# Kernel tuning notes

Hardware: AMD Instinct MI355X
Metric: run time of the kernel (lower is better)

Reference implementation:

```python
import jax, jax.numpy as jnp
import numpy as np

ALPHA = 1.702
LIMIT = 7.0


def setup_inputs() -> dict:
    E, H, D = 16, 2880, 2880
    B, S = 2, 1024
    T = B * S
    key = jax.random.key(0)
    ks = jax.random.split(key, 8)
    hidden_states = jax.random.normal(ks[0], (B, S, H), dtype=jnp.float32)
    routing_weights = jax.random.uniform(ks[1], (T, E), dtype=jnp.float32)
    scale = 0.02
    Wg = jax.random.normal(ks[2], (E, H, D), dtype=jnp.float32) * scale
    bg = jax.random.normal(ks[3], (E, D), dtype=jnp.float32) * scale
    Wu = jax.random.normal(ks[4], (E, H, D), dtype=jnp.float32) * scale
    bu = jax.random.normal(ks[5], (E, D), dtype=jnp.float32) * scale
    Wd = jax.random.normal(ks[6], (E, D, H), dtype=jnp.float32) * scale
    bd = jax.random.normal(ks[7], (E, H), dtype=jnp.float32) * scale
    return {"hidden_states": hidden_states, "routing_weights": routing_weights,
            "Wg": Wg, "bg": bg, "Wu": Wu, "bu": bu, "Wd": Wd, "bd": bd}


def reference(hidden_states, routing_weights, Wg, bg, Wu, bu, Wd, bd):
    orig_shape = hidden_states.shape
    H = Wg.shape[1]
    x = hidden_states.reshape(-1, H)  # [T, H]
    # per-expert gate/up projections: [E, T, D]
    gate = jnp.einsum('th,ehd->etd', x, Wg) + bg[:, None, :]
    gate = jnp.minimum(gate, LIMIT)
    up = jnp.einsum('th,ehd->etd', x, Wu) + bu[:, None, :]
    up = jnp.clip(up, -LIMIT, LIMIT)
    glu = gate * jax.nn.sigmoid(gate * ALPHA)
    inter = (up + 1.0) * glu  # [E, T, D]
    # down projection: [E, T, H]
    down = jnp.einsum('etd,edh->eth', inter, Wd) + bd[:, None, :]
    # routing-weighted sum over experts: [T, H]
    out = jnp.einsum('eth,te->th', down, routing_weights)
    return out.reshape(orig_shape)
```

## Files before the change

### kernel.cpp

```cpp
#include <hip/hip_runtime.h>
#include <cstdint>


#define ALPHA 1.702f
#define LIMIT 7.0f

static constexpr int E = 16;
static constexpr int H = 2880;
static constexpr int D = 2880;
static constexpr int T = 2048;
static constexpr int NKT = H / 64;
static constexpr int NG  = 4;

typedef float        f32x4  __attribute__((ext_vector_type(4)));
typedef short        bf16x8 __attribute__((ext_vector_type(8)));

#define MFMA_BF16(a,b,c) __builtin_amdgcn_mfma_f32_16x16x32_bf16((a),(b),(c),0,0,0)
#define SBAR()        __builtin_amdgcn_s_barrier()
#define SCHED_FENCE() __builtin_amdgcn_sched_barrier(0)

__device__ __forceinline__ unsigned short f2bf(float f){
  unsigned u = __builtin_bit_cast(unsigned, f);
  u += 0x7fffu + ((u >> 16) & 1u);
  return (unsigned short)(u >> 16);
}
__device__ __forceinline__ unsigned pack2(float a, float b){
  return (unsigned)f2bf(a) | ((unsigned)f2bf(b) << 16);
}

__device__ __forceinline__ void gload_lds16(const void* g, void* l){
  __builtin_amdgcn_global_load_lds((const __attribute__((address_space(1))) unsigned*)g,
                                   (__attribute__((address_space(3))) unsigned*)l,
                                   16, 0, 0);
}

__global__ void cvt_kernel(const float* __restrict__ in, unsigned short* __restrict__ ob, int n8){
  int i = blockIdx.x * 256 + threadIdx.x;
  if (i < n8){
    float4 a = ((const float4*)in)[2*i];
    float4 b = ((const float4*)in)[2*i+1];
    uint4 o;
    o.x = pack2(a.x, a.y); o.y = pack2(a.z, a.w);
    o.z = pack2(b.x, b.y); o.w = pack2(b.z, b.w);
    ((uint4*)ob)[i] = o;
  }
}

__global__ __launch_bounds__(256) void tcvt_kernel(
    const float* __restrict__ src, unsigned short* __restrict__ dst)
{
  __shared__ unsigned short tl[64*72];
  const int t = threadIdx.x;
  const size_t mo = (size_t)blockIdx.z * H * D;
  const int r0 = blockIdx.x * 64, c0 = blockIdx.y * 64;
  const float* s = src + mo;
  unsigned short* o = dst + mo;

  int rr = t >> 2;
  #pragma unroll
  for (int p = 0; p < 4; ++p){
    int cc = ((t & 3) + p*4) * 4;
    float4 v = *(const float4*)(s + (size_t)(r0 + rr)*D + c0 + cc);
    tl[(cc+0)*72 + rr] = f2bf(v.x);
    tl[(cc+1)*72 + rr] = f2bf(v.y);
    tl[(cc+2)*72 + rr] = f2bf(v.z);
    tl[(cc+3)*72 + rr] = f2bf(v.w);
  }
  __syncthreads();
  #pragma unroll
  for (int p = 0; p < 2; ++p){
    int task = p*256 + t;
    int cl = task >> 3, ch = task & 7;
    bf16x8 v = *(const bf16x8*)&tl[cl*72 + ch*8];
    *(bf16x8*)(o + (size_t)(c0 + cl)*H + r0 + ch*8) = v;
  }
}

__global__ void reduce_kernel(const float* __restrict__ p, float* __restrict__ out, int n4){
  int i = blockIdx.x * 256 + threadIdx.x;
  if (i < n4){
    f32x4 a = ((const f32x4*)p)[i];
    #pragma unroll
    for (int g = 1; g < NG; ++g)
      a += ((const f32x4*)(p + (size_t)g * T * H))[i];
    ((f32x4*)out)[i] = a;
  }
}

__global__ __launch_bounds__(256, 2) void gateup_kernel(
    const unsigned short* __restrict__ xb,
    const unsigned short* __restrict__ wgT,
    const float* __restrict__ bg,
    const unsigned short* __restrict__ wuT,
    const float* __restrict__ bu,
    unsigned short* __restrict__ inter,
    int e0)
{
  __shared__ short As[2][128*64];
  __shared__ short Bg[2][96*64];
  __shared__ short Bu[2][96*64];

  const int t = threadIdx.x, lane = t & 63, wv = t >> 6;
  const int wm = wv >> 1, wn = wv & 1;

  int nbx = gridDim.x, nby = gridDim.y;
  int lin = blockIdx.x + nbx*(blockIdx.y + nby*blockIdx.z);
  int per = (nbx*nby*gridDim.z) >> 3;
  int id2 = (lin & 7)*per + (lin >> 3);
  int bx = id2 % nbx; int rem = id2 / nbx;
  int by = rem % nby; int bz = rem / nby;

  const int trow0 = bx * 128, ncol0 = by * 96, ez = bz, e = e0 + ez;
  const unsigned short* wg = wgT + (size_t)ez * D * H;
  const unsigned short* wu = wuT + (size_t)ez * D * H;

  f32x4 accg[4][3], accu[4][3];
  #pragma unroll
  for (int i = 0; i < 4; ++i)
    #pragma unroll
    for (int j = 0; j < 3; ++j){
      accg[i][j] = (f32x4){0.f,0.f,0.f,0.f};
      accu[i][j] = (f32x4){0.f,0.f,0.f,0.f};
    }

  auto stage = [&](int kt, int buf){
    #pragma unroll
    for (int i = 0; i < 4; ++i){
      int task = i*256 + t, row = task >> 3, ch = task & 7, sch = ch ^ (row & 7);
      gload_lds16(xb + (size_t)(trow0 + row)*H + kt*64 + sch*8, &As[buf][task*8]);
    }
    #pragma unroll
    for (int j = 0; j < 3; ++j){
      int task = j*256 + t, row = task >> 3, ch = task & 7, sch = ch ^ (row & 7);
      size_t go = (size_t)(ncol0 + row)*H + kt*64 + sch*8;
      gload_lds16(wg + go, &Bg[buf][task*8]);
      gload_lds16(wu + go, &Bu[buf][task*8]);
    }
  };

  stage(0, 0);

  for (int kt = 0; kt < NKT; ++kt){
    int cur = kt & 1, nxt = cur ^ 1;
    int ktn = (kt+1 < NKT) ? kt+1 : kt;
    stage(ktn, nxt);
    asm volatile("s_waitcnt vmcnt(10)" ::: "memory");
    SCHED_FENCE(); SBAR(); SCHED_FENCE();
    #pragma unroll
    for (int kk = 0; kk < 2; ++kk){
      bf16x8 af[4];
      #pragma unroll
      for (int mi = 0; mi < 4; ++mi){
        int row = wm*64 + mi*16 + (lane & 15);
        int pc  = (kk*4 + (lane>>4)) ^ (row & 7);
        af[mi] = *(const bf16x8*)&As[cur][row*64 + pc*8];
      }
      bf16x8 fgv[3], fuv[3];
      #pragma unroll
      for (int ni = 0; ni < 3; ++ni){
        int row = (wn*3 + ni)*16 + (lane & 15);
        int pc  = (kk*4 + (lane>>4)) ^ (row & 7);
        fgv[ni] = *(const bf16x8*)&Bg[cur][row*64 + pc*8];
        fuv[ni] = *(const bf16x8*)&Bu[cur][row*64 + pc*8];
      }
      #pragma unroll
      for (int ni = 0; ni < 3; ++ni)
        #pragma unroll
        for (int mi = 0; mi < 4; ++mi){
          accg[mi][ni] = MFMA_BF16(af[mi], fgv[ni], accg[mi][ni]);
          accu[mi][ni] = MFMA_BF16(af[mi], fuv[ni], accu[mi][ni]);
        }
    }
    SBAR();
  }
  asm volatile("s_waitcnt vmcnt(0)" ::: "memory");

  const float* bgp = bg + (size_t)e * D;
  const float* bup = bu + (size_t)e * D;
  unsigned short* ip = inter + (size_t)ez * T * D;
  #pragma unroll
  for (int ni = 0; ni < 3; ++ni){
    int d = ncol0 + wn*48 + ni*16 + (lane & 15);
    float bgv = bgp[d], buv = bup[d];
    #pragma unroll
    for (int mi = 0; mi < 4; ++mi){
      #pragma unroll
      for (int r = 0; r < 4; ++r){
        int trw = trow0 + wm*64 + mi*16 + (lane >> 4)*4 + r;
        float g = accg[mi][ni][r] + bgv;
        float u = accu[mi][ni][r] + buv;
        g = fminf(g, LIMIT);
        u = fminf(fmaxf(u, -LIMIT), LIMIT);
        float glu = g / (1.f + __expf(-ALPHA * g));
        ip[(size_t)trw * D + d] = f2bf((u + 1.f) * glu);
      }
    }
  }
}

__global__ __launch_bounds__(256, 2) void down_kernel(
    const unsigned short* __restrict__ inter,
    const unsigned short* __restrict__ wdT,
    const float* __restrict__ bd,
    const float* __restrict__ rw,
    float* __restrict__ pout,
    int e0, int ec)
{
  __shared__ short As[2][128*64];
  __shared__ short Bs[2][192*64];

  const int t = threadIdx.x, lane = t & 63, wv = t >> 6;
  const int wm = wv >> 1, wn = wv & 1;

  int nbx = gridDim.x, nby = gridDim.y;
  int lin = blockIdx.x + nbx*(blockIdx.y + nby*blockIdx.z);
  int per = (nbx*nby*gridDim.z) >> 3;
  int id2 = (lin & 7)*per + (lin >> 3);
  int bx = id2 % nbx; int rem = id2 / nbx;
  int by = rem % nby; int g  = rem / nby;

  const int trow0 = bx * 128, ncol0 = by * 192;
  const int ne = (ec > g) ? ((ec - 1 - g) >> 2) + 1 : 0;

  f32x4 oacc[4][6];
  #pragma unroll
  for (int i = 0; i < 4; ++i)
    #pragma unroll
    for (int j = 0; j < 6; ++j) oacc[i][j] = (f32x4){0.f,0.f,0.f,0.f};

  auto stage = [&](int ee, int kt, int buf){
    const unsigned short* ap = inter + (size_t)ee * T * D;
    const unsigned short* wd = wdT + (size_t)ee * H * D;
    #pragma unroll
    for (int i = 0; i < 4; ++i){
      int task = i*256 + t, row = task >> 3, ch = task & 7, sch = ch ^ (row & 7);
      gload_lds16(ap + (size_t)(trow0 + row)*D + kt*64 + sch*8, &As[buf][task*8]);
    }
    #pragma unroll
    for (int j = 0; j < 6; ++j){
      int task = j*256 + t, row = task >> 3, ch = task & 7, sch = ch ^ (row & 7);
      gload_lds16(wd + (size_t)(ncol0 + row)*D + kt*64 + sch*8, &Bs[buf][task*8]);
    }
  };

  if (ne > 0){
    stage(g, 0, 0);

    int gkt = 0;
    for (int ei = 0; ei < ne; ++ei){
      const int ee = g + ei*4;
      const int e  = e0 + ee;
      f32x4 acc[4][6];
      #pragma unroll
      for (int i = 0; i < 4; ++i)
        #pragma unroll
        for (int j = 0; j < 6; ++j) acc[i][j] = (f32x4){0.f,0.f,0.f,0.f};

      for (int kt = 0; kt < NKT; ++kt, ++gkt){
        int cur = gkt & 1, nxt = cur ^ 1;
        int eeN, ktN;
        if (kt+1 < NKT)      { eeN = ee;     ktN = kt+1; }
        else if (ei+1 < ne)  { eeN = ee + 4; ktN = 0;    }
        else                 { eeN = ee;     ktN = kt;   }
        stage(eeN, ktN, nxt);
        asm volatile("s_waitcnt vmcnt(10)" ::: "memory");
        SCHED_FENCE(); SBAR(); SCHED_FENCE();
        #pragma unroll
        for (int kk = 0; kk < 2; ++kk){
          bf16x8 af[4];
          #pragma unroll
          for (int mi = 0; mi < 4; ++mi){
            int row = wm*64 + mi*16 + (lane & 15);
            int pc  = (kk*4 + (lane>>4)) ^ (row & 7);
            af[mi] = *(const bf16x8*)&As[cur][row*64 + pc*8];
          }
          bf16x8 fb[6];
          #pragma unroll
          for (int ni = 0; ni < 6; ++ni){
            int row = wn*96 + ni*16 + (lane & 15);
            int pc  = (kk*4 + (lane>>4)) ^ (row & 7);
            fb[ni] = *(const bf16x8*)&Bs[cur][row*64 + pc*8];
          }
          #pragma unroll
          for (int ni = 0; ni < 6; ++ni)
            #pragma unroll
            for (int mi = 0; mi < 4; ++mi)
              acc[mi][ni] = MFMA_BF16(af[mi], fb[ni], acc[mi][ni]);
        }
        SBAR();
      }

      const float* bdp = bd + (size_t)e * H;
      #pragma unroll
      for (int ni = 0; ni < 6; ++ni){
        int h = ncol0 + wn*96 + ni*16 + (lane & 15);
        float bdv = bdp[h];
        #pragma unroll
        for (int mi = 0; mi < 4; ++mi){
          #pragma unroll
          for (int r = 0; r < 4; ++r){
            int trw = trow0 + wm*64 + mi*16 + (lane >> 4)*4 + r;
            float rv = rw[trw*E + e];
            oacc[mi][ni][r] += rv * (acc[mi][ni][r] + bdv);
          }
        }
      }
    }
    asm volatile("s_waitcnt vmcnt(0)" ::: "memory");
  }

  float* pp = pout + (size_t)g * T * H;
  const int accum = (e0 != 0);
  #pragma unroll
  for (int ni = 0; ni < 6; ++ni){
    int h = ncol0 + wn*96 + ni*16 + (lane & 15);
    #pragma unroll
    for (int mi = 0; mi < 4; ++mi){
      #pragma unroll
      for (int r = 0; r < 4; ++r){
        int trw = trow0 + wm*64 + mi*16 + (lane >> 4)*4 + r;
        size_t oi = (size_t)trw * H + h;
        float v = oacc[mi][ni][r];
        if (accum) v += pp[oi];
        pp[oi] = v;
      }
    }
  }
}

extern "C" void kernel_launch(void* const* d_in, const int* in_sizes, int n_in,
                              void* d_out, int out_size, void* d_ws, size_t ws_size,
                              hipStream_t stream) {
  const float* hs  = (const float*)d_in[0];
  const float* rwt = (const float*)d_in[1];
  const float* Wg  = (const float*)d_in[2];
  const float* bg  = (const float*)d_in[3];
  const float* Wu  = (const float*)d_in[4];
  const float* bu  = (const float*)d_in[5];
  const float* Wd  = (const float*)d_in[6];
  const float* bd  = (const float*)d_in[7];
  float* out = (float*)d_out;

  const size_t xbytes = (size_t)T * H * 2;
  const size_t poutB  = (size_t)NG * T * H * 4;
  const size_t interB = (size_t)T * D * 2;
  const size_t wB     = (size_t)H * D * 2;
  const size_t perE   = interB + 2*wB;

  long long avail = (long long)ws_size - (long long)(xbytes + poutB);
  int EC = (int)(avail / (long long)perE);
  if (EC < 1) EC = 1;
  if (EC > E) EC = E;

  unsigned short* xb    = (unsigned short*)d_ws;
  float*          pout  = (float*)((char*)d_ws + xbytes);
  unsigned short* inter = (unsigned short*)((char*)d_ws + xbytes + poutB);
  unsigned short* wgT   = (unsigned short*)((char*)d_ws + xbytes + poutB + (size_t)EC*interB);
  unsigned short* wuT   = wgT + (size_t)EC * H * D;
  unsigned short* wdT   = wgT;

  cvt_kernel<<<(T*H/8 + 255)/256, 256, 0, stream>>>(hs, xb, T*H/8);

  for (int e0 = 0; e0 < E; e0 += EC){
    int ec = (E - e0 < EC) ? (E - e0) : EC;
    tcvt_kernel<<<dim3(45,45,ec), 256, 0, stream>>>(Wg + (size_t)e0*H*D, wgT);
    tcvt_kernel<<<dim3(45,45,ec), 256, 0, stream>>>(Wu + (size_t)e0*H*D, wuT);
    gateup_kernel<<<dim3(T/128, D/96, ec), 256, 0, stream>>>(xb, wgT, bg, wuT, bu, inter, e0);
    tcvt_kernel<<<dim3(45,45,ec), 256, 0, stream>>>(Wd + (size_t)e0*D*H, wdT);
    down_kernel<<<dim3(T/128, H/192, NG), 256, 0, stream>>>(inter, wdT, bd, rwt, pout, e0, ec);
  }
  reduce_kernel<<<(T*H/4 + 255)/256, 256, 0, stream>>>(pout, out, T*H/4);
}
```

Before: 2.265 ms.

## Enlarge MoE GEMM tiles, interleave gate/up weights, per-expert down partials

Both GEMM kernels move to 256x288 tiles with 6 waves (384 threads) and an 8x6 MFMA accumulator per wave, to raise operand reuse per LDS load. The gate and up weights are transposed into one interleaved matrix, so a single B tile carries matching gate and up columns and the epilogue pairs them. The down kernel now processes one expert per block and writes a routing-weighted partial into a per-expert buffer, and the final reduce sums all 16 buffers. The trade-off is a much larger partial-output workspace with extra reduce traffic, and about 136KB of LDS per block, which likely limits each CU to one resident block.

```diff
diff --git a/kernel.cpp b/kernel.cpp
--- a/kernel.cpp
+++ b/kernel.cpp
@@ -10,7 +10,6 @@
 static constexpr int D = 2880;
 static constexpr int T = 2048;
 static constexpr int NKT = H / 64;
-static constexpr int NG  = 4;
 
 typedef float        f32x4  __attribute__((ext_vector_type(4)));
 typedef short        bf16x8 __attribute__((ext_vector_type(8)));
@@ -47,14 +46,14 @@
 }
 
 __global__ __launch_bounds__(256) void tcvt_kernel(
-    const float* __restrict__ src, unsigned short* __restrict__ dst)
+    const float* __restrict__ src, unsigned short* __restrict__ dst,
+    int mode, size_t dstExpStride)
 {
   __shared__ unsigned short tl[64*72];
   const int t = threadIdx.x;
-  const size_t mo = (size_t)blockIdx.z * H * D;
+  const float* s = src + (size_t)blockIdx.z * H * D;
+  unsigned short* o = dst + (size_t)blockIdx.z * dstExpStride;
   const int r0 = blockIdx.x * 64, c0 = blockIdx.y * 64;
-  const float* s = src + mo;
-  unsigned short* o = dst + mo;
 
   int rr = t >> 2;
   #pragma unroll
@@ -71,8 +70,10 @@
   for (int p = 0; p < 2; ++p){
     int task = p*256 + t;
     int cl = task >> 3, ch = task & 7;
+    int c = c0 + cl;
+    int rowp = (mode < 2) ? ((c/48)*96 + (c%48) + mode*48) : c;
     bf16x8 v = *(const bf16x8*)&tl[cl*72 + ch*8];
-    *(bf16x8*)(o + (size_t)(c0 + cl)*H + r0 + ch*8) = v;
+    *(bf16x8*)(o + (size_t)rowp*H + r0 + ch*8) = v;
   }
 }
 
@@ -81,60 +82,55 @@
   if (i < n4){
     f32x4 a = ((const f32x4*)p)[i];
     #pragma unroll
-    for (int g = 1; g < NG; ++g)
+    for (int g = 1; g < E; ++g)
       a += ((const f32x4*)(p + (size_t)g * T * H))[i];
     ((f32x4*)out)[i] = a;
   }
 }
 
-__global__ __launch_bounds__(256, 2) void gateup_kernel(
+__global__ __launch_bounds__(384, 2) void gateup_kernel(
     const unsigned short* __restrict__ xb,
-    const unsigned short* __restrict__ wgT,
+    const unsigned short* __restrict__ wGU,
     const float* __restrict__ bg,
-    const unsigned short* __restrict__ wuT,
     const float* __restrict__ bu,
     unsigned short* __restrict__ inter,
     int e0)
 {
-  __shared__ short As[2][128*64];
-  __shared__ short Bg[2][96*64];
-  __shared__ short Bu[2][96*64];
+  __shared__ short As[2][256*64];
+  __shared__ short Bs[2][288*64];
 
   const int t = threadIdx.x, lane = t & 63, wv = t >> 6;
-  const int wm = wv >> 1, wn = wv & 1;
+  const int wm = wv / 3, wn = wv % 3;
 
   int nbx = gridDim.x, nby = gridDim.y;
   int lin = blockIdx.x + nbx*(blockIdx.y + nby*blockIdx.z);
   int per = (nbx*nby*gridDim.z) >> 3;
   int id2 = (lin & 7)*per + (lin >> 3);
   int bx = id2 % nbx; int rem = id2 / nbx;
-  int by = rem % nby; int bz = rem / nby;
-
-  const int trow0 = bx * 128, ncol0 = by * 96, ez = bz, e = e0 + ez;
-  const unsigned short* wg = wgT + (size_t)ez * D * H;
-  const unsigned short* wu = wuT + (size_t)ez * D * H;
-
-  f32x4 accg[4][3], accu[4][3];
-  #pragma unroll
-  for (int i = 0; i < 4; ++i)
-    #pragma unroll
-    for (int j = 0; j < 3; ++j){
-      accg[i][j] = (f32x4){0.f,0.f,0.f,0.f};
-      accu[i][j] = (f32x4){0.f,0.f,0.f,0.f};
-    }
+  int by = rem % nby; int ez = rem / nby;
+
+  const int trow0 = bx * 256, ncol0p = by * 288;
+  const int e = e0 + ez;
+  const unsigned short* wg = wGU + (size_t)ez * 2 * D * H;
+
+  f32x4 acc[8][6];
+  #pragma unroll
+  for (int i = 0; i < 8; ++i)
+    #pragma unroll
+    for (int j = 0; j < 6; ++j) acc[i][j] = (f32x4){0.f,0.f,0.f,0.f};
 
   auto stage = [&](int kt, int buf){
     #pragma unroll
-    for (int i = 0; i < 4; ++i){
-      int task = i*256 + t, row = task >> 3, ch = task & 7, sch = ch ^ (row & 7);
+    for (int r = 0; r < 6; ++r){
+      int task = (r < 5) ? (r*384 + t) : (1920 + (t & 127));
+      int row = task >> 3, ch = task & 7, sch = ch ^ (row & 7);
       gload_lds16(xb + (size_t)(trow0 + row)*H + kt*64 + sch*8, &As[buf][task*8]);
     }
     #pragma unroll
-    for (int j = 0; j < 3; ++j){
-      int task = j*256 + t, row = task >> 3, ch = task & 7, sch = ch ^ (row & 7);
-      size_t go = (size_t)(ncol0 + row)*H + kt*64 + sch*8;
-      gload_lds16(wg + go, &Bg[buf][task*8]);
-      gload_lds16(wu + go, &Bu[buf][task*8]);
+    for (int r = 0; r < 6; ++r){
+      int task = r*384 + t;
+      int row = task >> 3, ch = task & 7, sch = ch ^ (row & 7);
+      gload_lds16(wg + (size_t)(ncol0p + row)*H + kt*64 + sch*8, &Bs[buf][task*8]);
     }
   };
 
@@ -144,32 +140,26 @@
     int cur = kt & 1, nxt = cur ^ 1;
     int ktn = (kt+1 < NKT) ? kt+1 : kt;
     stage(ktn, nxt);
-    asm volatile("s_waitcnt vmcnt(10)" ::: "memory");
+    asm volatile("s_waitcnt vmcnt(12)" ::: "memory");
     SCHED_FENCE(); SBAR(); SCHED_FENCE();
     #pragma unroll
     for (int kk = 0; kk < 2; ++kk){
-      bf16x8 af[4];
-      #pragma unroll
-      for (int mi = 0; mi < 4; ++mi){
-        int row = wm*64 + mi*16 + (lane & 15);
+      bf16x8 af[8];
+      #pragma unroll
+      for (int mi = 0; mi < 8; ++mi){
+        int row = wm*128 + mi*16 + (lane & 15);
         int pc  = (kk*4 + (lane>>4)) ^ (row & 7);
         af[mi] = *(const bf16x8*)&As[cur][row*64 + pc*8];
       }
-      bf16x8 fgv[3], fuv[3];
-      #pragma unroll
-      for (int ni = 0; ni < 3; ++ni){
-        int row = (wn*3 + ni)*16 + (lane & 15);
-        int pc  = (kk*4 + (lane>>4)) ^ (row & 7);
-        fgv[ni] = *(const bf16x8*)&Bg[cur][row*64 + pc*8];
-        fuv[ni] = *(const bf16x8*)&Bu[cur][row*64 + pc*8];
-      }
-      #pragma unroll
-      for (int ni = 0; ni < 3; ++ni)
+      #pragma unroll
+      for (int ni = 0; ni < 6; ++ni){
+        int rowB = wn*96 + ni*16 + (lane & 15);
+        int pc   = (kk*4 + (lane>>4)) ^ (rowB & 7);
+        bf16x8 fb = *(const bf16x8*)&Bs[cur][rowB*64 + pc*8];
         #pragma unroll
-        for (int mi = 0; mi < 4; ++mi){
-          accg[mi][ni] = MFMA_BF16(af[mi], fgv[ni], accg[mi][ni]);
-          accu[mi][ni] = MFMA_BF16(af[mi], fuv[ni], accu[mi][ni]);
-        }
+        for (int mi = 0; mi < 8; ++mi)
+          acc[mi][ni] = MFMA_BF16(af[mi], fb, acc[mi][ni]);
+      }
     }
     SBAR();
   }
@@ -179,150 +169,121 @@
   const float* bup = bu + (size_t)e * D;
   unsigned short* ip = inter + (size_t)ez * T * D;
   #pragma unroll
-  for (int ni = 0; ni < 3; ++ni){
-    int d = ncol0 + wn*48 + ni*16 + (lane & 15);
+  for (int g = 0; g < 3; ++g){
+    int d = by*144 + wn*48 + g*16 + (lane & 15);
     float bgv = bgp[d], buv = bup[d];
     #pragma unroll
-    for (int mi = 0; mi < 4; ++mi){
+    for (int mi = 0; mi < 8; ++mi){
       #pragma unroll
       for (int r = 0; r < 4; ++r){
-        int trw = trow0 + wm*64 + mi*16 + (lane >> 4)*4 + r;
-        float g = accg[mi][ni][r] + bgv;
-        float u = accu[mi][ni][r] + buv;
-        g = fminf(g, LIMIT);
-        u = fminf(fmaxf(u, -LIMIT), LIMIT);
-        float glu = g / (1.f + __expf(-ALPHA * g));
-        ip[(size_t)trw * D + d] = f2bf((u + 1.f) * glu);
-      }
-    }
-  }
-}
-
-__global__ __launch_bounds__(256, 2) void down_kernel(
+        int trw = trow0 + wm*128 + mi*16 + (lane >> 4)*4 + r;
+        float gv = acc[mi][g][r] + bgv;
+        float uv = acc[mi][g+3][r] + buv;
+        gv = fminf(gv, LIMIT);
+        uv = fminf(fmaxf(uv, -LIMIT), LIMIT);
+        float glu = gv / (1.f + __expf(-ALPHA * gv));
+        ip[(size_t)trw * D + d] = f2bf((uv + 1.f) * glu);
+      }
+    }
+  }
+}
+
+__global__ __launch_bounds__(384, 2) void down_kernel(
     const unsigned short* __restrict__ inter,
     const unsigned short* __restrict__ wdT,
     const float* __restrict__ bd,
     const float* __restrict__ rw,
     float* __restrict__ pout,
-    int e0, int ec)
+    int e0)
 {
-  __shared__ short As[2][128*64];
-  __shared__ short Bs[2][192*64];
+  __shared__ short As[2][256*64];
+  __shared__ short Bs[2][288*64];
 
   const int t = threadIdx.x, lane = t & 63, wv = t >> 6;
-  const int wm = wv >> 1, wn = wv & 1;
+  const int wm = wv / 3, wn = wv % 3;
 
   int nbx = gridDim.x, nby = gridDim.y;
   int lin = blockIdx.x + nbx*(blockIdx.y + nby*blockIdx.z);
   int per = (nbx*nby*gridDim.z) >> 3;
   int id2 = (lin & 7)*per + (lin >> 3);
   int bx = id2 % nbx; int rem = id2 / nbx;
-  int by = rem % nby; int g  = rem / nby;
-
-  const int trow0 = bx * 128, ncol0 = by * 192;
-  const int ne = (ec > g) ? ((ec - 1 - g) >> 2) + 1 : 0;
-
-  f32x4 oacc[4][6];
-  #pragma unroll
-  for (int i = 0; i < 4; ++i)
-    #pragma unroll
-    for (int j = 0; j < 6; ++j) oacc[i][j] = (f32x4){0.f,0.f,0.f,0.f};
-
-  auto stage = [&](int ee, int kt, int buf){
-    const unsigned short* ap = inter + (size_t)ee * T * D;
-    const unsigned short* wd = wdT + (size_t)ee * H * D;
-    #pragma unroll
-    for (int i = 0; i < 4; ++i){
-      int task = i*256 + t, row = task >> 3, ch = task & 7, sch = ch ^ (row & 7);
+  int by = rem % nby; int ez = rem / nby;
+
+  const int trow0 = bx * 256, ncol0 = by * 288;
+  const int e = e0 + ez;
+  const unsigned short* ap = inter + (size_t)ez * T * D;
+  const unsigned short* wd = wdT + (size_t)ez * H * D;
+
+  f32x4 acc[8][6];
+  #pragma unroll
+  for (int i = 0; i < 8; ++i)
+    #pragma unroll
+    for (int j = 0; j < 6; ++j) acc[i][j] = (f32x4){0.f,0.f,0.f,0.f};
+
+  auto stage = [&](int kt, int buf){
+    #pragma unroll
+    for (int r = 0; r < 6; ++r){
+      int task = (r < 5) ? (r*384 + t) : (1920 + (t & 127));
+      int row = task >> 3, ch = task & 7, sch = ch ^ (row & 7);
       gload_lds16(ap + (size_t)(trow0 + row)*D + kt*64 + sch*8, &As[buf][task*8]);
     }
     #pragma unroll
-    for (int j = 0; j < 6; ++j){
-      int task = j*256 + t, row = task >> 3, ch = task & 7, sch = ch ^ (row & 7);
+    for (int r = 0; r < 6; ++r){
+      int task = r*384 + t;
+      int row = task >> 3, ch = task & 7, sch = ch ^ (row & 7);
       gload_lds16(wd + (size_t)(ncol0 + row)*D + kt*64 + sch*8, &Bs[buf][task*8]);
     }
   };
 
-  if (ne > 0){
-    stage(g, 0, 0);
-
-    int gkt = 0;
-    for (int ei = 0; ei < ne; ++ei){
-      const int ee = g + ei*4;
-      const int e  = e0 + ee;
-      f32x4 acc[4][6];
-      #pragma unroll
-      for (int i = 0; i < 4; ++i)
+  stage(0, 0);
+
+  for (int kt = 0; kt < NKT; ++kt){
+    int cur = kt & 1, nxt = cur ^ 1;
+    int ktn = (kt+1 < NKT) ? kt+1 : kt;
+    stage(ktn, nxt);
+    asm volatile("s_waitcnt vmcnt(12)" ::: "memory");
+    SCHED_FENCE(); SBAR(); SCHED_FENCE();
+    #pragma unroll
+    for (int kk = 0; kk < 2; ++kk){
+      bf16x8 af[8];
+      #pragma unroll
+      for (int mi = 0; mi < 8; ++mi){
+        int row = wm*128 + mi*16 + (lane & 15);
+        int pc  = (kk*4 + (lane>>4)) ^ (row & 7);
+        af[mi] = *(const bf16x8*)&As[cur][row*64 + pc*8];
+      }
+      #pragma unroll
+      for (int ni = 0; ni < 6; ++ni){
+        int rowB = wn*96 + ni*16 + (lane & 15);
+        int pc   = (kk*4 + (lane>>4)) ^ (rowB & 7);
+        bf16x8 fb = *(const bf16x8*)&Bs[cur][rowB*64 + pc*8];
         #pragma unroll
-        for (int j = 0; j < 6; ++j) acc[i][j] = (f32x4){0.f,0.f,0.f,0.f};
-
-      for (int kt = 0; kt < NKT; ++kt, ++gkt){
-        int cur = gkt & 1, nxt = cur ^ 1;
-        int eeN, ktN;
-        if (kt+1 < NKT)      { eeN = ee;     ktN = kt+1; }
-        else if (ei+1 < ne)  { eeN = ee + 4; ktN = 0;    }
-        else                 { eeN = ee;     ktN = kt;   }
-        stage(eeN, ktN, nxt);
-        asm volatile("s_waitcnt vmcnt(10)" ::: "memory");
-        SCHED_FENCE(); SBAR(); SCHED_FENCE();
-        #pragma unroll
-        for (int kk = 0; kk < 2; ++kk){
-          bf16x8 af[4];
-          #pragma unroll
-          for (int mi = 0; mi < 4; ++mi){
-            int row = wm*64 + mi*16 + (lane & 15);
-            int pc  = (kk*4 + (lane>>4)) ^ (row & 7);
-            af[mi] = *(const bf16x8*)&As[cur][row*64 + pc*8];
-          }
-          bf16x8 fb[6];
-          #pragma unroll
-          for (int ni = 0; ni < 6; ++ni){
-            int row = wn*96 + ni*16 + (lane & 15);
-            int pc  = (kk*4 + (lane>>4)) ^ (row & 7);
-            fb[ni] = *(const bf16x8*)&Bs[cur][row*64 + pc*8];
-          }
-          #pragma unroll
-          for (int ni = 0; ni < 6; ++ni)
-            #pragma unroll
-            for (int mi = 0; mi < 4; ++mi)
-              acc[mi][ni] = MFMA_BF16(af[mi], fb[ni], acc[mi][ni]);
-        }
-        SBAR();
-      }
-
-      const float* bdp = bd + (size_t)e * H;
-      #pragma unroll
-      for (int ni = 0; ni < 6; ++ni){
-        int h = ncol0 + wn*96 + ni*16 + (lane & 15);
-        float bdv = bdp[h];
-        #pragma unroll
-        for (int mi = 0; mi < 4; ++mi){
-          #pragma unroll
-          for (int r = 0; r < 4; ++r){
-            int trw = trow0 + wm*64 + mi*16 + (lane >> 4)*4 + r;
-            float rv = rw[trw*E + e];
-            oacc[mi][ni][r] += rv * (acc[mi][ni][r] + bdv);
-          }
-        }
-      }
-    }
-    asm volatile("s_waitcnt vmcnt(0)" ::: "memory");
-  }
-
-  float* pp = pout + (size_t)g * T * H;
-  const int accum = (e0 != 0);
+        for (int mi = 0; mi < 8; ++mi)
+          acc[mi][ni] = MFMA_BF16(af[mi], fb, acc[mi][ni]);
+      }
+    }
+    SBAR();
+  }
+  asm volatile("s_waitcnt vmcnt(0)" ::: "memory");
+
+  const float* bdp = bd + (size_t)e * H;
+  float* pp = pout + (size_t)e * T * H;
+  float rvv[8][4];
+  #pragma unroll
+  for (int mi = 0; mi < 8; ++mi)
+    #pragma unroll
+    for (int r = 0; r < 4; ++r)
+      rvv[mi][r] = rw[(trow0 + wm*128 + mi*16 + (lane>>4)*4 + r)*E + e];
   #pragma unroll
   for (int ni = 0; ni < 6; ++ni){
     int h = ncol0 + wn*96 + ni*16 + (lane & 15);
-    #pragma unroll
-    for (int mi = 0; mi < 4; ++mi){
+    float bdv = bdp[h];
+    #pragma unroll
+    for (int mi = 0; mi < 8; ++mi){
       #pragma unroll
       for (int r = 0; r < 4; ++r){
-        int trw = trow0 + wm*64 + mi*16 + (lane >> 4)*4 + r;
-        size_t oi = (size_t)trw * H + h;
-        float v = oacc[mi][ni][r];
-        if (accum) v += pp[oi];
-        pp[oi] = v;
+        int trw = trow0 + wm*128 + mi*16 + (lane >> 4)*4 + r;
+        pp[(size_t)trw * H + h] = rvv[mi][r] * (acc[mi][ni][r] + bdv);
       }
     }
   }
@@ -342,10 +303,10 @@
   float* out = (float*)d_out;
 
   const size_t xbytes = (size_t)T * H * 2;
-  const size_t poutB  = (size_t)NG * T * H * 4;
+  const size_t poutB  = (size_t)E * T * H * 4;
   const size_t interB = (size_t)T * D * 2;
-  const size_t wB     = (size_t)H * D * 2;
-  const size_t perE   = interB + 2*wB;
+  const size_t guB    = (size_t)2 * D * H * 2;
+  const size_t perE   = interB + guB;
 
   long long avail = (long long)ws_size - (long long)(xbytes + poutB);
   int EC = (int)(avail / (long long)perE);
@@ -355,19 +316,17 @@
   unsigned short* xb    = (unsigned short*)d_ws;
   float*          pout  = (float*)((char*)d_ws + xbytes);
   unsigned short* inter = (unsigned short*)((char*)d_ws + xbytes + poutB);
-  unsigned short* wgT   = (unsigned short*)((char*)d_ws + xbytes + poutB + (size_t)EC*interB);
-  unsigned short* wuT   = wgT + (size_t)EC * H * D;
-  unsigned short* wdT   = wgT;
+  unsigned short* wGU   = (unsigned short*)((char*)d_ws + xbytes + poutB + (size_t)EC*interB);
 
   cvt_kernel<<<(T*H/8 + 255)/256, 256, 0, stream>>>(hs, xb, T*H/8);
 
   for (int e0 = 0; e0 < E; e0 += EC){
     int ec = (E - e0 < EC) ? (E - e0) : EC;
-    tcvt_kernel<<<dim3(45,45,ec), 256, 0, stream>>>(Wg + (size_t)e0*H*D, wgT);
-    tcvt_kernel<<<dim3(45,45,ec), 256, 0, stream>>>(Wu + (size_t)e0*H*D, wuT);
-    gateup_kernel<<<dim3(T/128, D/96, ec), 256, 0, stream>>>(xb, wgT, bg, wuT, bu, inter, e0);
-    tcvt_kernel<<<dim3(45,45,ec), 256, 0, stream>>>(Wd + (size_t)e0*D*H, wdT);
-    down_kernel<<<dim3(T/128, H/192, NG), 256, 0, stream>>>(inter, wdT, bd, rwt, pout, e0, ec);
+    tcvt_kernel<<<dim3(45,45,ec), 256, 0, stream>>>(Wg + (size_t)e0*H*D, wGU, 0, (size_t)2*D*H);
+    tcvt_kernel<<<dim3(45,45,ec), 256, 0, stream>>>(Wu + (size_t)e0*H*D, wGU, 1, (size_t)2*D*H);
+    gateup_kernel<<<dim3(8, 20, ec), 384, 0, stream>>>(xb, wGU, bg, bu, inter, e0);
+    tcvt_kernel<<<dim3(45,45,ec), 256, 0, stream>>>(Wd + (size_t)e0*D*H, wGU, 2, (size_t)D*H);
+    down_kernel<<<dim3(8, 10, ec), 384, 0, stream>>>(inter, wGU, bd, rwt, pout, e0);
   }
   reduce_kernel<<<(T*H/4 + 255)/256, 256, 0, stream>>>(pout, out, T*H/4);
 }
```

Result: slower. 3.421 ms (+51.1%).

## Interleave global-to-LDS loads with MFMA phases and raise wave priority during compute

Applied to the files above, without the earlier changes.

Each K-step of both the gate/up and down GEMM kernels is split into four MFMA phases separated by barriers. The next tile's global-to-LDS loads are spread across those phases instead of being issued in one burst, and the wait drops from vmcnt(10) to vmcnt(3). s_setprio raises wave priority around the MFMA bursts, and explicit lgkmcnt waits fence the LDS fragment reads. The goal is to keep memory traffic overlapped with matrix work and to shrink issue stalls, at the cost of more barriers per K-step and tighter ordering assumptions on the staged loads.

```diff
diff --git a/kernel.cpp b/kernel.cpp
--- a/kernel.cpp
+++ b/kernel.cpp
@@ -18,6 +18,9 @@
 #define MFMA_BF16(a,b,c) __builtin_amdgcn_mfma_f32_16x16x32_bf16((a),(b),(c),0,0,0)
 #define SBAR()        __builtin_amdgcn_s_barrier()
 #define SCHED_FENCE() __builtin_amdgcn_sched_barrier(0)
+#define PRIO1()       __builtin_amdgcn_s_setprio(1)
+#define PRIO0()       __builtin_amdgcn_s_setprio(0)
+#define LGK0()        asm volatile("s_waitcnt lgkmcnt(0)" ::: "memory")
 
 __device__ __forceinline__ unsigned short f2bf(float f){
   unsigned u = __builtin_bit_cast(unsigned, f);
@@ -108,9 +111,10 @@
   int per = (nbx*nby*gridDim.z) >> 3;
   int id2 = (lin & 7)*per + (lin >> 3);
   int bx = id2 % nbx; int rem = id2 / nbx;
-  int by = rem % nby; int bz = rem / nby;
-
-  const int trow0 = bx * 128, ncol0 = by * 96, ez = bz, e = e0 + ez;
+  int by = rem % nby; int ez = rem / nby;
+
+  const int trow0 = bx * 128, ncol0 = by * 96;
+  const int e = e0 + ez;
   const unsigned short* wg = wgT + (size_t)ez * D * H;
   const unsigned short* wu = wuT + (size_t)ez * D * H;
 
@@ -123,55 +127,87 @@
       accu[i][j] = (f32x4){0.f,0.f,0.f,0.f};
     }
 
-  auto stage = [&](int kt, int buf){
-    #pragma unroll
-    for (int i = 0; i < 4; ++i){
-      int task = i*256 + t, row = task >> 3, ch = task & 7, sch = ch ^ (row & 7);
-      gload_lds16(xb + (size_t)(trow0 + row)*H + kt*64 + sch*8, &As[buf][task*8]);
-    }
-    #pragma unroll
-    for (int j = 0; j < 3; ++j){
-      int task = j*256 + t, row = task >> 3, ch = task & 7, sch = ch ^ (row & 7);
-      size_t go = (size_t)(ncol0 + row)*H + kt*64 + sch*8;
-      gload_lds16(wg + go, &Bg[buf][task*8]);
-      gload_lds16(wu + go, &Bu[buf][task*8]);
-    }
-  };
-
-  stage(0, 0);
+  auto sA = [&](int kt, int buf, int i){
+    int task = i*256 + t, row = task >> 3, ch = task & 7, sch = ch ^ (row & 7);
+    gload_lds16(xb + (size_t)(trow0 + row)*H + kt*64 + sch*8, &As[buf][task*8]);
+  };
+  auto sBg = [&](int kt, int buf, int j){
+    int task = j*256 + t, row = task >> 3, ch = task & 7, sch = ch ^ (row & 7);
+    gload_lds16(wg + (size_t)(ncol0 + row)*H + kt*64 + sch*8, &Bg[buf][task*8]);
+  };
+  auto sBu = [&](int kt, int buf, int j){
+    int task = j*256 + t, row = task >> 3, ch = task & 7, sch = ch ^ (row & 7);
+    gload_lds16(wu + (size_t)(ncol0 + row)*H + kt*64 + sch*8, &Bu[buf][task*8]);
+  };
+
+  auto readAf = [&](bf16x8* af, int cur, int kk){
+    #pragma unroll
+    for (int mi = 0; mi < 4; ++mi){
+      int row = wm*64 + mi*16 + (lane & 15);
+      int pc  = (kk*4 + (lane>>4)) ^ (row & 7);
+      af[mi] = *(const bf16x8*)&As[cur][row*64 + pc*8];
+    }
+  };
+  auto readF = [&](bf16x8* fr, const short* B, int kk){
+    #pragma unroll
+    for (int ni = 0; ni < 3; ++ni){
+      int row = (wn*3 + ni)*16 + (lane & 15);
+      int pc  = (kk*4 + (lane>>4)) ^ (row & 7);
+      fr[ni] = *(const bf16x8*)&B[row*64 + pc*8];
+    }
+  };
+
+  #pragma unroll
+  for (int i = 0; i < 4; ++i) sA(0, 0, i);
+  #pragma unroll
+  for (int j = 0; j < 3; ++j){ sBg(0, 0, j); sBu(0, 0, j); }
 
   for (int kt = 0; kt < NKT; ++kt){
     int cur = kt & 1, nxt = cur ^ 1;
     int ktn = (kt+1 < NKT) ? kt+1 : kt;
-    stage(ktn, nxt);
-    asm volatile("s_waitcnt vmcnt(10)" ::: "memory");
+    bf16x8 af[4], fr[3];
+    sA(ktn, nxt, 0); sA(ktn, nxt, 1); sA(ktn, nxt, 2);
+    asm volatile("s_waitcnt vmcnt(3)" ::: "memory");
     SCHED_FENCE(); SBAR(); SCHED_FENCE();
-    #pragma unroll
-    for (int kk = 0; kk < 2; ++kk){
-      bf16x8 af[4];
-      #pragma unroll
-      for (int mi = 0; mi < 4; ++mi){
-        int row = wm*64 + mi*16 + (lane & 15);
-        int pc  = (kk*4 + (lane>>4)) ^ (row & 7);
-        af[mi] = *(const bf16x8*)&As[cur][row*64 + pc*8];
-      }
-      bf16x8 fgv[3], fuv[3];
-      #pragma unroll
-      for (int ni = 0; ni < 3; ++ni){
-        int row = (wn*3 + ni)*16 + (lane & 15);
-        int pc  = (kk*4 + (lane>>4)) ^ (row & 7);
-        fgv[ni] = *(const bf16x8*)&Bg[cur][row*64 + pc*8];
-        fuv[ni] = *(const bf16x8*)&Bu[cur][row*64 + pc*8];
-      }
-      #pragma unroll
-      for (int ni = 0; ni < 3; ++ni)
-        #pragma unroll
-        for (int mi = 0; mi < 4; ++mi){
-          accg[mi][ni] = MFMA_BF16(af[mi], fgv[ni], accg[mi][ni]);
-          accu[mi][ni] = MFMA_BF16(af[mi], fuv[ni], accu[mi][ni]);
-        }
-    }
-    SBAR();
+    readAf(af, cur, 0); readF(fr, Bg[cur], 0);
+    LGK0(); SCHED_FENCE();
+    PRIO1();
+    #pragma unroll
+    for (int ni = 0; ni < 3; ++ni)
+      #pragma unroll
+      for (int mi = 0; mi < 4; ++mi)
+        accg[mi][ni] = MFMA_BF16(af[mi], fr[ni], accg[mi][ni]);
+    PRIO0(); SBAR();
+    sA(ktn, nxt, 3); sBg(ktn, nxt, 0); sBu(ktn, nxt, 0);
+    readF(fr, Bu[cur], 0);
+    LGK0(); SCHED_FENCE();
+    PRIO1();
+    #pragma unroll
+    for (int ni = 0; ni < 3; ++ni)
+      #pragma unroll
+      for (int mi = 0; mi < 4; ++mi)
+        accu[mi][ni] = MFMA_BF16(af[mi], fr[ni], accu[mi][ni]);
+    PRIO0(); SBAR();
+    sBg(ktn, nxt, 1); sBu(ktn, nxt, 1); sBg(ktn, nxt, 2);
+    readAf(af, cur, 1); readF(fr, Bg[cur], 1);
+    LGK0(); SCHED_FENCE();
+    PRIO1();
+    #pragma unroll
+    for (int ni = 0; ni < 3; ++ni)
+      #pragma unroll
+      for (int mi = 0; mi < 4; ++mi)
+        accg[mi][ni] = MFMA_BF16(af[mi], fr[ni], accg[mi][ni]);
+    PRIO0(); SBAR();
+    sBu(ktn, nxt, 2);
+    readF(fr, Bu[cur], 1);
+    LGK0(); SCHED_FENCE();
+    PRIO1();
+    #pragma unroll
+    for (int ni = 0; ni < 3; ++ni)
+      #pragma unroll
+      for (int mi = 0; mi < 4; ++mi)
+        accu[mi][ni] = MFMA_BF16(af[mi], fr[ni], accu[mi][ni]);
+    PRIO0(); SBAR();
   }
   asm volatile("s_waitcnt vmcnt(0)" ::: "memory");
 
@@ -228,23 +264,38 @@
     #pragma unroll
     for (int j = 0; j < 6; ++j) oacc[i][j] = (f32x4){0.f,0.f,0.f,0.f};
 
-  auto stage = [&](int ee, int kt, int buf){
-    const unsigned short* ap = inter + (size_t)ee * T * D;
-    const unsigned short* wd = wdT + (size_t)ee * H * D;
-    #pragma unroll
-    for (int i = 0; i < 4; ++i){
-      int task = i*256 + t, row = task >> 3, ch = task & 7, sch = ch ^ (row & 7);
-      gload_lds16(ap + (size_t)(trow0 + row)*D + kt*64 + sch*8, &As[buf][task*8]);
-    }
-    #pragma unroll
-    for (int j = 0; j < 6; ++j){
-      int task = j*256 + t, row = task >> 3, ch = task & 7, sch = ch ^ (row & 7);
-      gload_lds16(wd + (size_t)(ncol0 + row)*D + kt*64 + sch*8, &Bs[buf][task*8]);
+  auto sA = [&](const unsigned short* ap, int kt, int buf, int i){
+    int task = i*256 + t, row = task >> 3, ch = task & 7, sch = ch ^ (row & 7);
+    gload_lds16(ap + (size_t)(trow0 + row)*D + kt*64 + sch*8, &As[buf][task*8]);
+  };
+  auto sB = [&](const unsigned short* wd, int kt, int buf, int j){
+    int task = j*256 + t, row = task >> 3, ch = task & 7, sch = ch ^ (row & 7);
+    gload_lds16(wd + (size_t)(ncol0 + row)*D + kt*64 + sch*8, &Bs[buf][task*8]);
+  };
+  auto readAf = [&](bf16x8* af, int cur, int kk){
+    #pragma unroll
+    for (int mi = 0; mi < 4; ++mi){
+      int row = wm*64 + mi*16 + (lane & 15);
+      int pc  = (kk*4 + (lane>>4)) ^ (row & 7);
+      af[mi] = *(const bf16x8*)&As[cur][row*64 + pc*8];
+    }
+  };
+  auto readF3 = [&](bf16x8* fr, int cur, int kk, int nh){
+    #pragma unroll
+    for (int q = 0; q < 3; ++q){
+      int row = wn*96 + (nh*3 + q)*16 + (lane & 15);
+      int pc  = (kk*4 + (lane>>4)) ^ (row & 7);
+      fr[q] = *(const bf16x8*)&Bs[cur][row*64 + pc*8];
     }
   };
 
   if (ne > 0){
-    stage(g, 0, 0);
+    const unsigned short* ap0 = inter + (size_t)g * T * D;
+    const unsigned short* wd0 = wdT + (size_t)g * H * D;
+    #pragma unroll
+    for (int i = 0; i < 4; ++i) sA(ap0, 0, 0, i);
+    #pragma unroll
+    for (int j = 0; j < 6; ++j) sB(wd0, 0, 0, j);
 
     int gkt = 0;
     for (int ei = 0; ei < ne; ++ei){
@@ -262,32 +313,51 @@
         if (kt+1 < NKT)      { eeN = ee;     ktN = kt+1; }
         else if (ei+1 < ne)  { eeN = ee + 4; ktN = 0;    }
         else                 { eeN = ee;     ktN = kt;   }
-        stage(eeN, ktN, nxt);
-        asm volatile("s_waitcnt vmcnt(10)" ::: "memory");
+        const unsigned short* apN = inter + (size_t)eeN * T * D;
+        const unsigned short* wdN = wdT + (size_t)eeN * H * D;
+        bf16x8 af[4], fr[3];
+        sA(apN, ktN, nxt, 0); sA(apN, ktN, nxt, 1); sA(apN, ktN, nxt, 2);
+        asm volatile("s_waitcnt vmcnt(3)" ::: "memory");
         SCHED_FENCE(); SBAR(); SCHED_FENCE();
-        #pragma unroll
-        for (int kk = 0; kk < 2; ++kk){
-          bf16x8 af[4];
+        readAf(af, cur, 0); readF3(fr, cur, 0, 0);
+        LGK0(); SCHED_FENCE();
+        PRIO1();
+        #pragma unroll
+        for (int q = 0; q < 3; ++q)
           #pragma unroll
-          for (int mi = 0; mi < 4; ++mi){
-            int row = wm*64 + mi*16 + (lane & 15);
-            int pc  = (kk*4 + (lane>>4)) ^ (row & 7);
-            af[mi] = *(const bf16x8*)&As[cur][row*64 + pc*8];
-          }
-          bf16x8 fb[6];
+          for (int mi = 0; mi < 4; ++mi)
+            acc[mi][q] = MFMA_BF16(af[mi], fr[q], acc[mi][q]);
+        PRIO0(); SBAR();
+        sA(apN, ktN, nxt, 3); sB(wdN, ktN, nxt, 0); sB(wdN, ktN, nxt, 1);
+        readF3(fr, cur, 0, 1);
+        LGK0(); SCHED_FENCE();
+        PRIO1();
+        #pragma unroll
+        for (int q = 0; q < 3; ++q)
           #pragma unroll
-          for (int ni = 0; ni < 6; ++ni){
-            int row = wn*96 + ni*16 + (lane & 15);
-            int pc  = (kk*4 + (lane>>4)) ^ (row & 7);
-            fb[ni] = *(const bf16x8*)&Bs[cur][row*64 + pc*8];
-          }
+          for (int mi = 0; mi < 4; ++mi)
+            acc[mi][3+q] = MFMA_BF16(af[mi], fr[q], acc[mi][3+q]);
+        PRIO0(); SBAR();
+        sB(wdN, ktN, nxt, 2); sB(wdN, ktN, nxt, 3); sB(wdN, ktN, nxt, 4);
+        readAf(af, cur, 1); readF3(fr, cur, 1, 0);
+        LGK0(); SCHED_FENCE();
+        PRIO1();
+        #pragma unroll
+        for (int q = 0; q < 3; ++q)
           #pragma unroll
-          for (int ni = 0; ni < 6; ++ni)
-            #pragma unroll
-            for (int mi = 0; mi < 4; ++mi)
-              acc[mi][ni] = MFMA_BF16(af[mi], fb[ni], acc[mi][ni]);
-        }
-        SBAR();
+          for (int mi = 0; mi < 4; ++mi)
+            acc[mi][q] = MFMA_BF16(af[mi], fr[q], acc[mi][q]);
+        PRIO0(); SBAR();
+        sB(wdN, ktN, nxt, 5);
+        readF3(fr, cur, 1, 1);
+        LGK0(); SCHED_FENCE();
+        PRIO1();
+        #pragma unroll
+        for (int q = 0; q < 3; ++q)
+          #pragma unroll
+          for (int mi = 0; mi < 4; ++mi)
+            acc[mi][3+q] = MFMA_BF16(af[mi], fr[q], acc[mi][3+q]);
+        PRIO0(); SBAR();
       }
 
       const float* bdp = bd + (size_t)e * H;
@@ -366,7 +436,7 @@
     tcvt_kernel<<<dim3(45,45,ec), 256, 0, stream>>>(Wg + (size_t)e0*H*D, wgT);
     tcvt_kernel<<<dim3(45,45,ec), 256, 0, stream>>>(Wu + (size_t)e0*H*D, wuT);
     gateup_kernel<<<dim3(T/128, D/96, ec), 256, 0, stream>>>(xb, wgT, bg, wuT, bu, inter, e0);
-    tcvt_kernel<<<dim3(45,45,ec), 256, 0, stream>>>(Wd + (size_t)e0*D*H, wdT);
+    tcvt_kernel<<<dim3(45,45,ec), 256, 0, stream>>>(Wd + (size_t)e0*D*H, wgT);
     down_kernel<<<dim3(T/128, H/192, NG), 256, 0, stream>>>(inter, wdT, bd, rwt, pout, e0, ec);
   }
   reduce_kernel<<<(T*H/4 + 255)/256, 256, 0, stream>>>(pout, out, T*H/4);
```

New measurement: 3.537 ms. 1.56x slower.
